# Optimization experiments

Hardware: AMD Instinct MI355X
Metric: run time of the kernel (lower is better)

## Reference

```python
import jax, jax.numpy as jnp
import numpy as np

N_CANDIDATE_K = 10
CENTER_RADIUS = 2.5
STRIDE = 32.0
ALPHA, GAMMA = 0.25, 2.0


def cxcywh_to_xyxy(b):
    cx, cy, w, h = b[..., 0], b[..., 1], b[..., 2], b[..., 3]
    return jnp.stack([cx - 0.5 * w, cy - 0.5 * h, cx + 0.5 * w, cy + 0.5 * h], axis=-1)


def box_iou_xyxy(a, b):
    # a: [Q,4], b: [G,4] -> iou [Q,G], union [Q,G]
    area_a = (a[:, 2] - a[:, 0]) * (a[:, 3] - a[:, 1])
    area_b = (b[:, 2] - b[:, 0]) * (b[:, 3] - b[:, 1])
    lt = jnp.maximum(a[:, None, :2], b[None, :, :2])
    rb = jnp.minimum(a[:, None, 2:], b[None, :, 2:])
    wh = jnp.clip(rb - lt, 0.0)
    inter = wh[..., 0] * wh[..., 1]
    union = area_a[:, None] + area_b[None, :] - inter
    return inter / union, union


def generalized_box_iou(a, b):
    iou, union = box_iou_xyxy(a, b)
    lt = jnp.minimum(a[:, None, :2], b[None, :, :2])
    rb = jnp.maximum(a[:, None, 2:], b[None, :, 2:])
    wh = jnp.clip(rb - lt, 0.0)
    enclose = wh[..., 0] * wh[..., 1]
    return iou - (enclose - union) / enclose


def in_boxes_info(boxes, gts):
    # boxes: [Q,4] cxcywh, gts: [G,4] cxcywh
    xy = cxcywh_to_xyxy(gts)  # [G,4]
    ax = boxes[:, 0:1]  # [Q,1]
    ay = boxes[:, 1:2]
    in_box = (ax > xy[:, 0]) & (ax < xy[:, 2]) & (ay > xy[:, 1]) & (ay < xy[:, 3])  # [Q,G]
    r = CENTER_RADIUS / STRIDE
    in_ctr = (ax > gts[:, 0] - r) & (ax < gts[:, 0] + r) & (ay > gts[:, 1] - r) & (ay < gts[:, 1] + r)
    fg_mask = in_box.any(axis=1) | in_ctr.any(axis=1)  # [Q]
    return fg_mask, in_box & in_ctr


def build_cost(prob, boxes, labels, gt_boxes):
    # prob [Q,C], boxes [Q,4], labels [G] int, gt_boxes [G,4] -> cost [Q,G], ious [Q,G]
    fg_mask, iibc = in_boxes_info(boxes, gt_boxes)
    bx = cxcywh_to_xyxy(boxes)
    gx = cxcywh_to_xyxy(gt_boxes)
    ious, _ = box_iou_xyxy(bx, gx)
    p = prob[:, labels]  # gather per-gt class prob -> [Q,G]
    neg = (1.0 - ALPHA) * p ** GAMMA * (-jnp.log1p(-(p - 1e-8) - 1.0 + 1.0) if False else -jnp.log(1.0 - p + 1e-8))
    pos = ALPHA * (1.0 - p) ** GAMMA * (-jnp.log(p + 1e-8))
    cost_class = pos - neg
    cost_giou = -generalized_box_iou(bx, gx)
    cost = cost_class + 3.0 * cost_giou + 100.0 * (1.0 - iibc.astype(cost_class.dtype))
    cost = cost + 10000.0 * (1.0 - fg_mask.astype(cost.dtype))[:, None]
    return cost, ious


def dynamic_k_matching(cost, ious):
    Q, G = cost.shape
    # dynamic k per gt from sum of top-10 ious (truncated to int, min 1)
    topk_ious, _ = jax.lax.top_k(ious.T, N_CANDIDATE_K)  # [G,10]
    dyn_k = jnp.maximum(topk_ious.sum(-1).astype(jnp.int32), 1)  # [G]
    # per-gt lowest-cost topk via rank matrix (rank of each query in ascending cost)
    ranks = jnp.argsort(jnp.argsort(cost, axis=0), axis=0)
    matching = (ranks < dyn_k[None, :]).astype(cost.dtype)  # [Q,G]
    # resolve anchors matched to >1 gt: keep only their argmin-cost gt
    anchor_matching_gt = matching.sum(axis=1)
    stale_mask = anchor_matching_gt > 1  # (reused stale inside while loop, as in torch source)
    row_argmin = jnp.argmin(cost, axis=1)
    onehot = jax.nn.one_hot(row_argmin, G, dtype=matching.dtype)
    matching = jnp.where(stale_mask[:, None], onehot, matching)
    qids = jnp.arange(Q)

    def cond(state):
        _, m = state
        return (m.sum(axis=0) == 0).any()

    def body(state):
        c, m = state
        pred = (m.sum(axis=0) == 0).any()  # gate for vmap safety
        matched_q = m.sum(axis=1) > 0
        c2 = c + 100000.0 * matched_q[:, None].astype(c.dtype)
        unmatched = m.sum(axis=0) == 0
        col_argmin = jnp.argmin(c2, axis=0)  # [G]
        add = (qids[:, None] == col_argmin[None, :]) & unmatched[None, :]
        m2 = jnp.where(add, jnp.asarray(1.0, c.dtype), m)
        fix = (m2.sum(axis=1) > 1).any()
        row_am = jnp.argmin(c2, axis=1)
        oh = jax.nn.one_hot(row_am, G, dtype=m2.dtype)
        m3 = jnp.where(fix & stale_mask[:, None], oh, m2)
        return (jnp.where(pred, c2, c), jnp.where(pred, m3, m))

    cost_f, matching = jax.lax.while_loop(cond, body, (cost, matching))
    selected_query = matching.sum(axis=1) > 0  # [Q] bool
    gt_assign = jnp.argmax(matching, axis=1).astype(jnp.int32)  # [Q], valid where selected
    masked_cost = jnp.where(matching > 0, cost_f, jnp.inf)
    matched_query_id = jnp.argmin(masked_cost, axis=0).astype(jnp.int32)  # [G]
    return selected_query, gt_assign, matched_query_id


def reference(pred_logits, pred_boxes, tgt_labels, tgt_boxes):
    prob = jax.nn.sigmoid(pred_logits)

    def per_image(p, b, l, g):
        cost, ious = build_cost(p, b, l, g)
        return dynamic_k_matching(cost, ious)

    return jax.vmap(per_image)(prob, pred_boxes, tgt_labels, tgt_boxes)


def setup_inputs() -> dict:
    key = jax.random.key(0)
    B, Q, C, G = 16, 8400, 80, 64
    k1, k2, k3, k4 = jax.random.split(key, 4)

    def make_boxes(kk, shape):
        ka, kb = jax.random.split(kk)
        cxcy = jax.random.uniform(ka, shape + (2,), minval=0.1, maxval=0.9, dtype=jnp.float32)
        wh = jax.random.uniform(kb, shape + (2,), minval=0.05, maxval=0.3, dtype=jnp.float32)
        return jnp.concatenate([cxcy, wh], axis=-1)

    return {
        "pred_logits": jax.random.normal(k1, (B, Q, C), dtype=jnp.float32),
        "pred_boxes": make_boxes(k2, (B, Q)),
        "tgt_labels": jax.random.randint(k3, (B, G), 0, C),
        "tgt_boxes": make_boxes(k4, (B, G)),
    }
```

## Files before the change

### kernel.cpp

```cpp
#include <hip/hip_runtime.h>
#include <cstdint>
#include <cstddef>


static constexpr int Bn = 16;
static constexpr int Qn = 8400;
static constexpr int Cn = 80;
static constexpr int Gn = 64;
#define TPB 512
#define MLIST_CAP 1536
#define STALE_CAP 320
#define QT 128

__device__ __forceinline__ unsigned int ordf(float f) {
    unsigned int u = __float_as_uint(f);
    return u ^ ((unsigned int)((int)u >> 31) | 0x80000000u);
}
__device__ __forceinline__ float inv_ordf(unsigned int o) {
    unsigned int u = (o & 0x80000000u) ? (o ^ 0x80000000u) : ~o;
    return __uint_as_float(u);
}
__device__ __forceinline__ float replay_penalty(float v, unsigned int k) {
    for (unsigned int t = 0; t < k; ++t) v += 100000.0f;
    return v;
}

__global__ __launch_bounds__(QT)
void build_cost_kernel(const float* __restrict__ logits,
                       const float* __restrict__ pboxes,
                       const int*   __restrict__ labels,
                       const float* __restrict__ gboxes,
                       float* __restrict__ cost_cm,
                       float* __restrict__ ious_cm,
                       unsigned char* __restrict__ rowarg)
{
    const int b = blockIdx.y;
    const int q0 = blockIdx.x * QT;
    const int tid = threadIdx.x;
    const int q = q0 + tid;
    const int qmax = (Qn - q0 < QT) ? (Qn - q0) : QT;

    __shared__ float sl[QT*81];
    __shared__ float gx0[Gn], gy0[Gn], gx1[Gn], gy1[Gn];
    __shared__ float gcx[Gn], gcy[Gn], gar[Gn];
    __shared__ int   glab[Gn];

    if (tid < Gn) {
        int g = tid;
        const float* gb = &gboxes[((size_t)b*Gn + g)*4];
        float cx = gb[0], cy = gb[1], w = gb[2], h = gb[3];
        float x0 = cx - 0.5f*w, y0 = cy - 0.5f*h;
        float x1 = cx + 0.5f*w, y1 = cy + 0.5f*h;
        gx0[g]=x0; gy0[g]=y0; gx1[g]=x1; gy1[g]=y1;
        gcx[g]=cx; gcy[g]=cy;
        gar[g]=(x1-x0)*(y1-y0);
        glab[g]=labels[(size_t)b*Gn + g];
    }
    for (int i = tid; i < QT*20; i += QT) {
        int row = i / 20, c4 = i % 20;
        if (row < qmax) {
            const float4 v = *(const float4*)&logits[((size_t)b*Qn + q0 + row)*Cn + c4*4];
            float* d = &sl[row*81 + c4*4];
            d[0]=v.x; d[1]=v.y; d[2]=v.z; d[3]=v.w;
        }
    }
    __syncthreads();
    if (tid >= qmax) return;

    const float* pb = &pboxes[((size_t)b*Qn + q)*4];
    float cx = pb[0], cy = pb[1], w = pb[2], h = pb[3];
    float ax0 = cx - 0.5f*w, ay0 = cy - 0.5f*h;
    float ax1 = cx + 0.5f*w, ay1 = cy + 0.5f*h;
    float areaA = (ax1-ax0)*(ay1-ay0);
    const float r = 2.5f/32.0f;

    bool anyBox=false, anyCtr=false;
    for (int g=0; g<Gn; ++g) {
        bool ib = (cx>gx0[g]) && (cx<gx1[g]) && (cy>gy0[g]) && (cy<gy1[g]);
        bool ic = (cx>gcx[g]-r) && (cx<gcx[g]+r) && (cy>gcy[g]-r) && (cy<gcy[g]+r);
        anyBox |= ib; anyCtr |= ic;
    }
    float fgterm = (anyBox || anyCtr) ? 0.0f : 10000.0f;

    float rmin = __builtin_inff(); int rarg = 0;
    size_t obase = ((size_t)b*Gn)*Qn + q;
    const float* myrow = &sl[tid*81];
    for (int g=0; g<Gn; ++g) {
        float X0=gx0[g], Y0=gy0[g], X1=gx1[g], Y1=gy1[g];
        float ltx=fmaxf(ax0,X0), lty=fmaxf(ay0,Y0);
        float rbx=fminf(ax1,X1), rby=fminf(ay1,Y1);
        float wx=fmaxf(rbx-ltx,0.f), wy=fmaxf(rby-lty,0.f);
        float inter=wx*wy;
        float uni=(areaA+gar[g])-inter;
        float iou=inter/uni;
        float l2x=fminf(ax0,X0), l2y=fminf(ay0,Y0);
        float r2x=fmaxf(ax1,X1), r2y=fmaxf(ay1,Y1);
        float ex=fmaxf(r2x-l2x,0.f), ey=fmaxf(r2y-l2y,0.f);
        float enc=ex*ey;
        float giou = iou - (enc-uni)/enc;
        float xlg = myrow[glab[g]];
        float p = 1.0f/(1.0f+expf(-xlg));
        float neg = 0.75f*(p*p)*(-logf(1.0f-p+1e-8f));
        float pos = 0.25f*((1.0f-p)*(1.0f-p))*(-logf(p+1e-8f));
        float cls = pos - neg;
        bool ib = (cx>X0)&&(cx<X1)&&(cy>Y0)&&(cy<Y1);
        bool ic = (cx>gcx[g]-r)&&(cx<gcx[g]+r)&&(cy>gcy[g]-r)&&(cy<gcy[g]+r);
        float iibc = (ib&&ic) ? 1.0f : 0.0f;
        float cost = ((cls + 3.0f*(-giou)) + 100.0f*(1.0f-iibc)) + fgterm;
        cost_cm[obase + (size_t)g*Qn] = cost;
        ious_cm[obase + (size_t)g*Qn] = iou;
        if (cost < rmin) { rmin = cost; rarg = g; }
    }
    rowarg[(size_t)b*Qn + q] = (unsigned char)rarg;
}

__device__ __forceinline__ void hist_find(unsigned int* hist, unsigned int* chunk,
                                          unsigned int* s_bin, unsigned int* s_cb,
                                          unsigned int want, int tid)
{
    if (tid < 64) {
        unsigned int s = 0;
        for (int i = 0; i < 64; ++i) s += hist[tid*64 + i];
        chunk[tid] = s;
    }
    __syncthreads();
    if (tid == 0) {
        unsigned int acc = 0; int c = 0;
        for (; c < 63; ++c) { if (acc + chunk[c] >= want) break; acc += chunk[c]; }
        int bbase = c*64; unsigned int bb = 0;
        for (; bb < 63; ++bb) { unsigned int h = hist[bbase+bb]; if (acc + h >= want) break; acc += h; }
        *s_bin = (unsigned int)(bbase + bb);
        *s_cb  = acc;
    }
    __syncthreads();
}

__global__ __launch_bounds__(512)
void column_select_kernel(const float* __restrict__ cost_all,
                          const float* __restrict__ ious_all,
                          int*   __restrict__ dynk_all,
                          float* __restrict__ poolv_all,
                          int*   __restrict__ poolq_all)
{
    const int g = blockIdx.x, b = blockIdx.y, tid = threadIdx.x;
    const float* ccol = cost_all + ((size_t)b*Gn + g)*Qn;
    const float* icol = ious_all + ((size_t)b*Gn + g)*Qn;

    __shared__ __align__(16) char u_smem[50048];
    __shared__ unsigned int chunk[64];
    __shared__ unsigned int s_bin1, s_bin2, s_bin3, s_cb1, s_cb2, s_cb3;
    __shared__ unsigned int s_nb, s_nt;
    __shared__ float pv[64]; __shared__ int pq[64];
    __shared__ float sv[64]; __shared__ int sq[64];
    __shared__ int tq[64];

    {
        float (*tl)[10] = (float(*)[10])u_smem;
        float tv[10];
        #pragma unroll
        for (int i=0;i<10;i++) tv[i] = -1.0f;
        for (int j=tid; j<Qn; j+=512) {
            float v = icol[j];
            if (v > tv[9]) {
                int k = 9;
                #pragma unroll
                for (int s=9; s>0; --s) { if (v > tv[s-1]) { tv[s]=tv[s-1]; k=s-1; } }
                tv[k]=v;
            }
        }
        #pragma unroll
        for (int i=0;i<10;i++) tl[tid][i]=tv[i];
        __syncthreads();
        for (int s=256; s>0; s>>=1) {
            if (tid < s) {
                float a[10], c[10];
                #pragma unroll
                for (int i=0;i<10;i++){ a[i]=tl[tid][i]; c[i]=tl[tid+s][i]; }
                float m[10]; int ia=0, ic=0;
                #pragma unroll
                for (int i=0;i<10;i++) {
                    float va = a[ia], vc = c[ic];
                    if (va >= vc) { m[i]=va; ++ia; } else { m[i]=vc; ++ic; }
                }
                #pragma unroll
                for (int i=0;i<10;i++) tl[tid][i]=m[i];
            }
            __syncthreads();
        }
        if (tid == 0) {
            float s = 0.0f;
            #pragma unroll
            for (int i=0;i<10;i++) s += tl[0][i];
            int k = (int)s;
            if (k < 1) k = 1;
            if (k > 10) k = 10;
            dynk_all[b*Gn + g] = k;
        }
    }
    __syncthreads();

    {
        unsigned int* s_ord = (unsigned int*)u_smem;
        unsigned int* hist  = (unsigned int*)(u_smem + 33664);
        const unsigned int want = 64;

        for (int i=tid;i<4096;i+=512) hist[i]=0u;
        __syncthreads();
        for (int j=tid;j<Qn;j+=512) {
            unsigned int od = ordf(ccol[j]);
            s_ord[j] = od;
            atomicAdd(&hist[od>>20],1u);
        }
        __syncthreads();
        hist_find(hist, chunk, &s_bin1, &s_cb1, want, tid);

        for (int i=tid;i<4096;i+=512) hist[i]=0u;
        __syncthreads();
        for (int j=tid;j<Qn;j+=512) {
            unsigned int od = s_ord[j];
            if ((od>>20)==s_bin1) atomicAdd(&hist[(od>>8)&0xFFFu],1u);
        }
        __syncthreads();
        hist_find(hist, chunk, &s_bin2, &s_cb2, want - s_cb1, tid);

        for (int i=tid;i<4096;i+=512) hist[i]=0u;
        __syncthreads();
        unsigned int hi24 = (s_bin1<<12) | s_bin2;
        for (int j=tid;j<Qn;j+=512) {
            unsigned int od = s_ord[j];
            if ((od>>8)==hi24) atomicAdd(&hist[od&0xFFu],1u);
        }
        __syncthreads();
        hist_find(hist, chunk, &s_bin3, &s_cb3, want - s_cb1 - s_cb2, tid);

        const unsigned int thr = (s_bin1<<20) | (s_bin2<<8) | s_bin3;
        const unsigned int c_strict = s_cb1 + s_cb2 + s_cb3;
        const unsigned int t_take = want - c_strict;
        if (tid==0) { s_nb=0u; s_nt=0u; }
        __syncthreads();
        for (int j=tid;j<Qn;j+=512) {
            unsigned int od = s_ord[j];
            if (od < thr) {
                unsigned int pos = atomicAdd(&s_nb,1u);
                if (pos < 64u) { pv[pos]=inv_ordf(od); pq[pos]=j; }
            } else if (od == thr) {
                unsigned int pos = atomicAdd(&s_nt,1u);
                if (pos < 64u) tq[pos]=j;
            }
        }
        __syncthreads();
        if (tid==0) {
            float thrv = inv_ordf(thr);
            int nt = (int)s_nt; if (nt > 64) nt = 64;
            for (int i=1;i<nt;++i){ int x=tq[i]; int k=i; while(k>0 && tq[k-1]>x){tq[k]=tq[k-1];--k;} tq[k]=x; }
            for (unsigned int r=0; r<t_take && (int)r<nt; ++r) { pv[c_strict+r]=thrv; pq[c_strict+r]=tq[r]; }
        }
        __syncthreads();
        if (tid < 64) {
            float v = pv[tid]; int qq = pq[tid];
            int rank = 0;
            for (int j=0;j<64;++j) {
                float u = pv[j]; int uq = pq[j];
                if (u < v || (u==v && uq<qq)) ++rank;
            }
            sv[rank]=v; sq[rank]=qq;
        }
        __syncthreads();
        if (tid < 64) {
            size_t base = ((size_t)b*Gn + g)*64 + tid;
            poolv_all[base] = sv[tid];
            poolq_all[base] = sq[tid];
        }
    }
}

__global__ __launch_bounds__(TPB)
void match_kernel(const float* __restrict__ cost_all,
                  const unsigned char* __restrict__ rowarg_all,
                  const int*   __restrict__ dynk_all,
                  const float* __restrict__ poolv_all,
                  const int*   __restrict__ poolq_all,
                  unsigned long long* __restrict__ mmask_all,
                  int* __restrict__ out)
{
    const int b = blockIdx.x;
    const int tid = threadIdx.x;
    const float* costb = cost_all + (size_t)b*Gn*Qn;
    const unsigned char* rarg = rowarg_all + (size_t)b*Qn;
    unsigned long long* mmask = mmask_all + (size_t)b*Qn;

    __shared__ __align__(16) unsigned long long s_pool_raw[2048];
    __shared__ int s_pq[Gn*64];
    __shared__ unsigned short s_kcnt[Qn];
    __shared__ int s_mlist[MLIST_CAP];
    __shared__ int s_staleq[STALE_CAP], s_stalec[STALE_CAP];
    __shared__ float s_mv[TPB]; __shared__ int s_mi[TPB];
    __shared__ int s_dynk[Gn];
    __shared__ unsigned int s_colcnt[Gn];
    __shared__ int s_winq[Gn];
    __shared__ unsigned long long s_unm, s_fbmask;
    __shared__ int s_mn, s_scnt, s_fix;

    float* s_pv = (float*)s_pool_raw;

    for (int q=tid; q<Qn; q+=TPB) s_kcnt[q]=0;
    for (int i=tid; i<Gn*64; i+=TPB) {
        size_t base = (size_t)b*Gn*64 + i;
        s_pv[i] = poolv_all[base];
        s_pq[i] = poolq_all[base];
    }
    if (tid < Gn) { s_dynk[tid] = dynk_all[b*Gn+tid]; s_colcnt[tid]=0u; }
    for (int q=tid; q<Qn; q+=TPB) mmask[q]=0ull;
    if (tid==0) { s_mn=0; s_scnt=0; s_fix=0; }
    __syncthreads();

    if (tid < Gn) {
        int k = s_dynk[tid];
        unsigned long long bit = 1ull<<tid;
        for (int t=0; t<k; ++t) {
            int q = s_pq[tid*64 + t];
            unsigned long long old = atomicOr(&mmask[q], bit);
            if (old == 0ull) {
                int pos = atomicAdd(&s_mn,1);
                if (pos < MLIST_CAP) s_mlist[pos]=q;
            }
        }
    }
    __syncthreads();
    int mn = s_mn; if (mn > MLIST_CAP) mn = MLIST_CAP;

    for (int j=tid; j<mn; j+=TPB) {
        int q = s_mlist[j];
        unsigned long long m = atomicOr(&mmask[q], 0ull);
        if (__popcll(m) > 1) {
            int pos = atomicAdd(&s_scnt,1);
            int rp = rarg[q];
            if (pos < STALE_CAP) { s_staleq[pos]=q; s_stalec[pos]=rp; }
            atomicExch(&mmask[q], 1ull<<rp);
        }
    }
    __syncthreads();
    const int scnt = (s_scnt < STALE_CAP) ? s_scnt : STALE_CAP;
    for (int j=tid; j<mn; j+=TPB) {
        unsigned long long m = atomicOr(&mmask[s_mlist[j]], 0ull);
        while (m) { int gg = __ffsll(m)-1; m &= m-1ull; atomicAdd(&s_colcnt[gg],1u); }
    }
    __syncthreads();

    for (int iter=0; iter<1024; ++iter) {
        if (tid < 64) {
            unsigned long long bal = __ballot(s_colcnt[tid]==0u);
            if (tid==0) { s_unm = bal; s_fbmask = 0ull; }
        }
        __syncthreads();
        const unsigned long long unm = s_unm;
        if (unm == 0ull) break;
        mn = s_mn; if (mn > MLIST_CAP) mn = MLIST_CAP;

        for (int j=tid; j<mn; j+=TPB) s_kcnt[s_mlist[j]]++;
        __syncthreads();

        int wq = -1;
        if (tid < 64 && ((unm>>tid)&1ull)) {
            for (int t=0; t<64; ++t) {
                int q = s_pq[tid*64 + t];
                if (s_kcnt[q]==0) { wq=q; break; }
            }
            if (wq < 0) atomicOr(&s_fbmask, 1ull<<tid);
        }
        __syncthreads();
        unsigned long long fb = s_fbmask;
        while (fb) {
            int c = __ffsll(fb)-1; fb &= fb-1ull;
            float bv=__builtin_inff(); int bq=0x7fffffff;
            for (int j=tid; j<Qn; j+=TPB) {
                if (s_kcnt[j]==0) {
                    float v = costb[(size_t)c*Qn + j];
                    if (v<bv || (v==bv && j<bq)) { bv=v; bq=j; }
                }
            }
            s_mv[tid]=bv; s_mi[tid]=bq;
            __syncthreads();
            for (int s=TPB/2; s>0; s>>=1) {
                if (tid<s) {
                    float v2=s_mv[tid+s]; int q2=s_mi[tid+s];
                    if (v2<s_mv[tid] || (v2==s_mv[tid] && q2<s_mi[tid])) { s_mv[tid]=v2; s_mi[tid]=q2; }
                }
                __syncthreads();
            }
            if (tid==0) s_winq[c]=s_mi[0];
            __syncthreads();
        }
        if (tid<64 && wq<0 && ((unm>>tid)&1ull)) wq = s_winq[tid];

        if (tid<64 && ((unm>>tid)&1ull) && wq>=0 && wq<Qn) {
            unsigned long long bit = 1ull<<tid;
            unsigned long long old = atomicOr(&mmask[wq], bit);
            if (old==0ull) {
                int pos = atomicAdd(&s_mn,1);
                if (pos < MLIST_CAP) s_mlist[pos]=wq;
            }
            if (__popcll(old|bit) > 1) s_fix = 1;
            atomicAdd(&s_colcnt[tid],1u);
        }
        __syncthreads();

        if (s_fix) {
            for (int j=tid; j<scnt; j+=TPB) {
                int q = s_staleq[j];
                unsigned int kk = s_kcnt[q];
                float best=__builtin_inff(); int bg=0;
                for (int gg=0; gg<Gn; ++gg) {
                    float v = replay_penalty(costb[(size_t)gg*Qn + q], kk);
                    if (v < best) { best=v; bg=gg; }
                }
                int oc = s_stalec[j];
                if (bg != oc) {
                    atomicAdd(&s_colcnt[oc], (unsigned int)-1);
                    atomicAdd(&s_colcnt[bg], 1u);
                    s_stalec[j] = bg;
                    atomicExch(&mmask[q], 1ull<<bg);
                }
            }
        }
        __syncthreads();
    }

    __syncthreads();
    mn = s_mn; if (mn > MLIST_CAP) mn = MLIST_CAP;
    unsigned long long* s_mcache = s_pool_raw;
    for (int j=tid; j<mn; j+=TPB) s_mcache[j] = atomicOr(&mmask[s_mlist[j]], 0ull);
    for (int q=tid; q<Qn; q+=TPB) {
        out[(size_t)b*Qn + q] = 0;
        out[(size_t)Bn*Qn + (size_t)b*Qn + q] = 0;
    }
    __syncthreads();
    for (int j=tid; j<mn; j+=TPB) {
        int q = s_mlist[j];
        unsigned long long m = s_mcache[j];
        out[(size_t)b*Qn + q] = 1;
        out[(size_t)Bn*Qn + (size_t)b*Qn + q] = __ffsll(m)-1;
    }
    __syncthreads();
    {
        const int g = tid>>3, p = tid&7;
        float best=__builtin_inff(); int bq=0x7fffffff;
        for (int j=p; j<mn; j+=8) {
            unsigned long long m = s_mcache[j];
            if ((m>>g)&1ull) {
                int q = s_mlist[j];
                float v = replay_penalty(costb[(size_t)g*Qn+q], s_kcnt[q]);
                if (v<best || (v==best && q<bq)) { best=v; bq=q; }
            }
        }
        s_mv[tid]=best; s_mi[tid]=bq;
    }
    __syncthreads();
    if (tid < Gn) {
        float best=__builtin_inff(); int bq=0x7fffffff;
        #pragma unroll
        for (int u=0;u<8;++u) {
            float v=s_mv[tid*8+u]; int qq=s_mi[tid*8+u];
            if (v<best || (v==best && qq<bq)) { best=v; bq=qq; }
        }
        if (bq>=Qn) bq=0;
        out[(size_t)2*Bn*Qn + (size_t)b*Gn + tid] = bq;
    }
}

extern "C" void kernel_launch(void* const* d_in, const int* in_sizes, int n_in,
                              void* d_out, int out_size, void* d_ws, size_t ws_size,
                              hipStream_t stream)
{
    const float* logits = (const float*)d_in[0];
    const float* pboxes = (const float*)d_in[1];
    const int*   labels = (const int*)d_in[2];
    const float* gboxes = (const float*)d_in[3];
    int* out = (int*)d_out;

    char* ws = (char*)d_ws;
    size_t off = 0;
    float* cost_cm = (float*)(ws + off); off += (size_t)Bn*Gn*Qn*sizeof(float);
    float* ious_cm = (float*)(ws + off); off += (size_t)Bn*Gn*Qn*sizeof(float);
    unsigned long long* mmask = (unsigned long long*)(ws + off); off += (size_t)Bn*Qn*sizeof(unsigned long long);
    float* poolv = (float*)(ws + off); off += (size_t)Bn*Gn*64*sizeof(float);
    int*   poolq = (int*)(ws + off);   off += (size_t)Bn*Gn*64*sizeof(int);
    int*   dynk  = (int*)(ws + off);   off += (size_t)Bn*Gn*sizeof(int);
    unsigned char* rowarg = (unsigned char*)(ws + off); off += (size_t)Bn*Qn;

    dim3 g1((Qn + QT - 1)/QT, Bn);
    build_cost_kernel<<<g1, QT, 0, stream>>>(logits, pboxes, labels, gboxes,
                                             cost_cm, ious_cm, rowarg);
    dim3 g2(Gn, Bn);
    column_select_kernel<<<g2, 512, 0, stream>>>(cost_cm, ious_cm, dynk, poolv, poolq);
    match_kernel<<<Bn, TPB, 0, stream>>>(cost_cm, rowarg, dynk, poolv, poolq, mmask, out);
}
```

Measured before the change: 323.2 us.

## Split class-cost gather into own kernel and recompute IoU in column select

Moves the sigmoid/focal class-cost computation into a separate gather kernel that writes a column-major class-cost buffer. The build-cost kernel then reads that buffer, caches the in-box-and-center test as a 64-bit mask, and stops writing the IoU matrix. Column select recomputes IoU from the box coordinates instead of reading it back. The aim is to cut the large IoU write and read and raise occupancy of the cost kernel, at the cost of an extra kernel launch and an extra full-size class-cost write and read.

```diff
diff --git a/kernel.cpp b/kernel.cpp
--- a/kernel.cpp
+++ b/kernel.cpp
@@ -10,7 +10,6 @@
 #define TPB 512
 #define MLIST_CAP 1536
 #define STALE_CAP 320
-#define QT 128
 
 __device__ __forceinline__ unsigned int ordf(float f) {
     unsigned int u = __float_as_uint(f);
@@ -25,28 +24,54 @@
     return v;
 }
 
-__global__ __launch_bounds__(QT)
-void build_cost_kernel(const float* __restrict__ logits,
-                       const float* __restrict__ pboxes,
+__global__ __launch_bounds__(256)
+void gather_cls_kernel(const float* __restrict__ logits,
                        const int*   __restrict__ labels,
+                       float* __restrict__ cls_cm)
+{
+    const int b = blockIdx.y;
+    const int q0 = blockIdx.x * 64;
+    const int tid = threadIdx.x;
+    const int qmax = (Qn - q0 < 64) ? (Qn - q0) : 64;
+
+    __shared__ float sl[64][81];
+    __shared__ int glab[Gn];
+    if (tid < Gn) glab[tid] = labels[b*Gn + tid];
+    for (int i = tid; i < 64*20; i += 256) {
+        int row = i / 20, c4 = i % 20;
+        if (row < qmax) {
+            const float4 v = *(const float4*)&logits[((size_t)b*Qn + q0 + row)*Cn + c4*4];
+            float* d = &sl[row][c4*4];
+            d[0]=v.x; d[1]=v.y; d[2]=v.z; d[3]=v.w;
+        }
+    }
+    __syncthreads();
+    for (int j = tid; j < Gn*64; j += 256) {
+        int g = j >> 6, qq = j & 63;
+        if (qq < qmax) {
+            float xlg = sl[qq][glab[g]];
+            float p = 1.0f/(1.0f+expf(-xlg));
+            float neg = 0.75f*(p*p)*(-logf(1.0f-p+1e-8f));
+            float pos = 0.25f*((1.0f-p)*(1.0f-p))*(-logf(p+1e-8f));
+            cls_cm[((size_t)b*Gn + g)*Qn + q0 + qq] = pos - neg;
+        }
+    }
+}
+
+__global__ __launch_bounds__(256)
+void build_cost_kernel(const float* __restrict__ pboxes,
                        const float* __restrict__ gboxes,
+                       const float* __restrict__ cls_cm,
                        float* __restrict__ cost_cm,
-                       float* __restrict__ ious_cm,
                        unsigned char* __restrict__ rowarg)
 {
     const int b = blockIdx.y;
-    const int q0 = blockIdx.x * QT;
-    const int tid = threadIdx.x;
-    const int q = q0 + tid;
-    const int qmax = (Qn - q0 < QT) ? (Qn - q0) : QT;
-
-    __shared__ float sl[QT*81];
+    const int q = blockIdx.x * 256 + threadIdx.x;
+
     __shared__ float gx0[Gn], gy0[Gn], gx1[Gn], gy1[Gn];
     __shared__ float gcx[Gn], gcy[Gn], gar[Gn];
-    __shared__ int   glab[Gn];
-
-    if (tid < Gn) {
-        int g = tid;
+    if (threadIdx.x < Gn) {
+        int g = threadIdx.x;
         const float* gb = &gboxes[((size_t)b*Gn + g)*4];
         float cx = gb[0], cy = gb[1], w = gb[2], h = gb[3];
         float x0 = cx - 0.5f*w, y0 = cy - 0.5f*h;
@@ -54,37 +79,29 @@
         gx0[g]=x0; gy0[g]=y0; gx1[g]=x1; gy1[g]=y1;
         gcx[g]=cx; gcy[g]=cy;
         gar[g]=(x1-x0)*(y1-y0);
-        glab[g]=labels[(size_t)b*Gn + g];
-    }
-    for (int i = tid; i < QT*20; i += QT) {
-        int row = i / 20, c4 = i % 20;
-        if (row < qmax) {
-            const float4 v = *(const float4*)&logits[((size_t)b*Qn + q0 + row)*Cn + c4*4];
-            float* d = &sl[row*81 + c4*4];
-            d[0]=v.x; d[1]=v.y; d[2]=v.z; d[3]=v.w;
-        }
-    }
-    __syncthreads();
-    if (tid >= qmax) return;
-
-    const float* pb = &pboxes[((size_t)b*Qn + q)*4];
-    float cx = pb[0], cy = pb[1], w = pb[2], h = pb[3];
+    }
+    __syncthreads();
+    if (q >= Qn) return;
+
+    const float4 pb = *(const float4*)&pboxes[((size_t)b*Qn + q)*4];
+    float cx = pb.x, cy = pb.y, w = pb.z, h = pb.w;
     float ax0 = cx - 0.5f*w, ay0 = cy - 0.5f*h;
     float ax1 = cx + 0.5f*w, ay1 = cy + 0.5f*h;
     float areaA = (ax1-ax0)*(ay1-ay0);
     const float r = 2.5f/32.0f;
 
+    unsigned long long ibc = 0ull;
     bool anyBox=false, anyCtr=false;
     for (int g=0; g<Gn; ++g) {
         bool ib = (cx>gx0[g]) && (cx<gx1[g]) && (cy>gy0[g]) && (cy<gy1[g]);
         bool ic = (cx>gcx[g]-r) && (cx<gcx[g]+r) && (cy>gcy[g]-r) && (cy<gcy[g]+r);
         anyBox |= ib; anyCtr |= ic;
+        if (ib && ic) ibc |= (1ull<<g);
     }
     float fgterm = (anyBox || anyCtr) ? 0.0f : 10000.0f;
 
     float rmin = __builtin_inff(); int rarg = 0;
     size_t obase = ((size_t)b*Gn)*Qn + q;
-    const float* myrow = &sl[tid*81];
     for (int g=0; g<Gn; ++g) {
         float X0=gx0[g], Y0=gy0[g], X1=gx1[g], Y1=gy1[g];
         float ltx=fmaxf(ax0,X0), lty=fmaxf(ay0,Y0);
@@ -98,17 +115,10 @@
         float ex=fmaxf(r2x-l2x,0.f), ey=fmaxf(r2y-l2y,0.f);
         float enc=ex*ey;
         float giou = iou - (enc-uni)/enc;
-        float xlg = myrow[glab[g]];
-        float p = 1.0f/(1.0f+expf(-xlg));
-        float neg = 0.75f*(p*p)*(-logf(1.0f-p+1e-8f));
-        float pos = 0.25f*((1.0f-p)*(1.0f-p))*(-logf(p+1e-8f));
-        float cls = pos - neg;
-        bool ib = (cx>X0)&&(cx<X1)&&(cy>Y0)&&(cy<Y1);
-        bool ic = (cx>gcx[g]-r)&&(cx<gcx[g]+r)&&(cy>gcy[g]-r)&&(cy<gcy[g]+r);
-        float iibc = (ib&&ic) ? 1.0f : 0.0f;
+        float cls = cls_cm[obase + (size_t)g*Qn];
+        float iibc = ((ibc>>g)&1ull) ? 1.0f : 0.0f;
         float cost = ((cls + 3.0f*(-giou)) + 100.0f*(1.0f-iibc)) + fgterm;
         cost_cm[obase + (size_t)g*Qn] = cost;
-        ious_cm[obase + (size_t)g*Qn] = iou;
         if (cost < rmin) { rmin = cost; rarg = g; }
     }
     rowarg[(size_t)b*Qn + q] = (unsigned char)rarg;
@@ -137,14 +147,14 @@
 
 __global__ __launch_bounds__(512)
 void column_select_kernel(const float* __restrict__ cost_all,
-                          const float* __restrict__ ious_all,
+                          const float* __restrict__ pboxes,
+                          const float* __restrict__ gboxes,
                           int*   __restrict__ dynk_all,
                           float* __restrict__ poolv_all,
                           int*   __restrict__ poolq_all)
 {
     const int g = blockIdx.x, b = blockIdx.y, tid = threadIdx.x;
     const float* ccol = cost_all + ((size_t)b*Gn + g)*Qn;
-    const float* icol = ious_all + ((size_t)b*Gn + g)*Qn;
 
     __shared__ __align__(16) char u_smem[50048];
     __shared__ unsigned int chunk[64];
@@ -155,12 +165,27 @@
     __shared__ int tq[64];
 
     {
+        const float* gb = &gboxes[((size_t)b*Gn + g)*4];
+        float gcx_=gb[0], gcy_=gb[1], gw=gb[2], gh=gb[3];
+        float X0=gcx_-0.5f*gw, Y0=gcy_-0.5f*gh, X1=gcx_+0.5f*gw, Y1=gcy_+0.5f*gh;
+        float garea=(X1-X0)*(Y1-Y0);
+        const float4* pb4 = (const float4*)(pboxes + (size_t)b*Qn*4);
+
         float (*tl)[10] = (float(*)[10])u_smem;
         float tv[10];
         #pragma unroll
         for (int i=0;i<10;i++) tv[i] = -1.0f;
         for (int j=tid; j<Qn; j+=512) {
-            float v = icol[j];
+            float4 pb = pb4[j];
+            float ax0=pb.x-0.5f*pb.z, ay0=pb.y-0.5f*pb.w;
+            float ax1=pb.x+0.5f*pb.z, ay1=pb.y+0.5f*pb.w;
+            float areaA=(ax1-ax0)*(ay1-ay0);
+            float ltx=fmaxf(ax0,X0), lty=fmaxf(ay0,Y0);
+            float rbx=fminf(ax1,X1), rby=fminf(ay1,Y1);
+            float wx=fmaxf(rbx-ltx,0.f), wy=fmaxf(rby-lty,0.f);
+            float inter=wx*wy;
+            float uni=(areaA+garea)-inter;
+            float v=inter/uni;
             if (v > tv[9]) {
                 int k = 9;
                 #pragma unroll
@@ -481,17 +506,20 @@
     char* ws = (char*)d_ws;
     size_t off = 0;
     float* cost_cm = (float*)(ws + off); off += (size_t)Bn*Gn*Qn*sizeof(float);
-    float* ious_cm = (float*)(ws + off); off += (size_t)Bn*Gn*Qn*sizeof(float);
+    float* cls_cm  = (float*)(ws + off); off += (size_t)Bn*Gn*Qn*sizeof(float);
     unsigned long long* mmask = (unsigned long long*)(ws + off); off += (size_t)Bn*Qn*sizeof(unsigned long long);
     float* poolv = (float*)(ws + off); off += (size_t)Bn*Gn*64*sizeof(float);
     int*   poolq = (int*)(ws + off);   off += (size_t)Bn*Gn*64*sizeof(int);
     int*   dynk  = (int*)(ws + off);   off += (size_t)Bn*Gn*sizeof(int);
     unsigned char* rowarg = (unsigned char*)(ws + off); off += (size_t)Bn*Qn;
 
-    dim3 g1((Qn + QT - 1)/QT, Bn);
-    build_cost_kernel<<<g1, QT, 0, stream>>>(logits, pboxes, labels, gboxes,
-                                             cost_cm, ious_cm, rowarg);
+    dim3 g0((Qn + 63)/64, Bn);
+    gather_cls_kernel<<<g0, 256, 0, stream>>>(logits, labels, cls_cm);
+    dim3 g1((Qn + 255)/256, Bn);
+    build_cost_kernel<<<g1, 256, 0, stream>>>(pboxes, gboxes, cls_cm,
+                                              cost_cm, rowarg);
     dim3 g2(Gn, Bn);
-    column_select_kernel<<<g2, 512, 0, stream>>>(cost_cm, ious_cm, dynk, poolv, poolq);
+    column_select_kernel<<<g2, 512, 0, stream>>>(cost_cm, pboxes, gboxes,
+                                                 dynk, poolv, poolq);
     match_kernel<<<Bn, TPB, 0, stream>>>(cost_cm, rowarg, dynk, poolv, poolq, mmask, out);
 }
```

Result: faster. 274.9 us (-14.9%).
